# Performance work log

Measured on AMD Instinct MI355X. Metric: run time of the kernel, lower is better.

Reference implementation:

```python
import jax, jax.numpy as jnp
import numpy as np

NUM_ENT = 50000
NUM_REL = 200          # init_rel has 2*NUM_REL rows (fwd + inverse)
D = 200                # init_dim = gcn_dim = embed_dim
B = 1024
E_HALF = 250000        # edges per direction; total 2*E_HALF
PERM = 1
K_H, K_W = 20, 10      # 2*k_w*k_h == 2*embed_dim
NUM_FILT = 96
KER = 9
FLAT_SZ = K_H * 2 * K_W * NUM_FILT * PERM  # 38400


def _bn(x, g, b, axes):
    # batch-norm with batch statistics (training-mode math, no running stats)
    m = jnp.mean(x, axes, keepdims=True)
    v = jnp.var(x, axes, keepdims=True)
    return (x - m) * jax.lax.rsqrt(v + 1e-5) * g + b


def setup_inputs() -> dict:
    key = jax.random.key(0)
    ks = jax.random.split(key, 24)
    rng = np.random.default_rng(0)
    # graph (constants)
    s = jax.random.randint(ks[0], (E_HALF,), 0, NUM_ENT)
    d = jax.random.randint(ks[1], (E_HALF,), 0, NUM_ENT)
    t = jax.random.randint(ks[2], (E_HALF,), 0, NUM_REL)
    edge_index = jnp.stack([jnp.concatenate([s, d]), jnp.concatenate([d, s])])  # [2, 2*E_HALF]
    edge_type = jnp.concatenate([t, t + NUM_REL])
    chequer_perm = jnp.asarray(np.stack([rng.permutation(2 * D) for _ in range(PERM)]), dtype=jnp.int32)
    # batch indices
    sub = jax.random.randint(ks[3], (B,), 0, NUM_ENT)
    rel = jax.random.randint(ks[4], (B,), 0, 2 * NUM_REL)
    neg_ents = jax.random.randint(ks[5], (B,), 0, NUM_ENT)
    n = lambda k, shp, sc=0.05: jax.random.normal(ks[k], shp, jnp.float32) * sc
    return {
        'sub': sub, 'rel': rel, 'neg_ents': neg_ents,
        'edge_index': edge_index, 'edge_type': edge_type, 'chequer_perm': chequer_perm,
        'init_embed': n(6, (NUM_ENT, D)),
        'init_rel': n(7, (2 * NUM_REL, D)),
        'w_in': n(8, (D, D)), 'w_out': n(9, (D, D)), 'w_loop': n(10, (D, D)),
        'w_rel': n(11, (D, D)), 'loop_rel': n(12, (1, D)),
        'bn0_g': jnp.ones((PERM,)), 'bn0_b': jnp.zeros((PERM,)),
        'bn1_g': jnp.ones((NUM_FILT * PERM,)), 'bn1_b': jnp.zeros((NUM_FILT * PERM,)),
        'bn2_g': jnp.ones((D,)), 'bn2_b': jnp.zeros((D,)),
        'conv_filt': n(13, (NUM_FILT, 1, KER, KER), 0.1),
        'fc_w': n(14, (D, FLAT_SZ), 0.01), 'fc_b': jnp.zeros((D,)),
        'bias_ent': jnp.zeros((NUM_ENT,)),
    }


def _forward(init_embed, init_rel, w_in, w_out, w_loop, w_rel, loop_rel,
             bn0_g, bn0_b, bn1_g, bn1_b, bn2_g, bn2_b,
             conv_filt, fc_w, fc_b, bias_ent,
             sub, rel, edge_index, edge_type, chequer_perm):
    # ---- GPKGConv encoder (CompGCN-style, op='sub', eval mode -> dropout off) ----
    src, dst = edge_index[0], edge_index[1]
    msg = init_embed[src] - init_rel[edge_type]                      # [E, D] irregular gather
    msg = jnp.concatenate([msg[:E_HALF] @ w_in, msg[E_HALF:] @ w_out], axis=0)
    deg = jax.ops.segment_sum(jnp.ones(msg.shape[0], msg.dtype), dst, num_segments=NUM_ENT)
    dinv = jnp.where(deg > 0, jax.lax.rsqrt(jnp.maximum(deg, 1.0)), 0.0)
    norm = (dinv[src] * dinv[dst])[:, None]
    agg = jax.ops.segment_sum(msg * norm, dst, num_segments=NUM_ENT)  # irregular scatter
    loop_msg = (init_embed - loop_rel) @ w_loop
    all_ent = jnp.tanh((agg + loop_msg) / 3.0)                        # [num_ent, D]
    r = init_rel @ w_rel                                              # [2*num_rel, D]
    # ---- InteractE-style chequer conv decoder ----
    sub_emb = all_ent[sub]
    rel_emb = r[rel]
    comb = jnp.concatenate([sub_emb, rel_emb], axis=1)                # [B, 2D]
    cheq = jnp.take(comb, chequer_perm, axis=1)                       # [B, perm, 2D]
    x = cheq.reshape(-1, PERM, 2 * K_W, K_H)
    x = _bn(x, bn0_g.reshape(1, -1, 1, 1), bn0_b.reshape(1, -1, 1, 1), (0, 2, 3))
    pad = KER // 2
    x = jnp.pad(x, ((0, 0), (0, 0), (pad, pad), (pad, pad)), mode='wrap')  # circular pad
    filt = jnp.tile(conv_filt, (PERM, 1, 1, 1))
    x = jax.lax.conv_general_dilated(x, filt, (1, 1), 'VALID',
                                     dimension_numbers=('NCHW', 'OIHW', 'NCHW'),
                                     feature_group_count=PERM)        # [B, 96, 20, 20]
    x = _bn(x, bn1_g.reshape(1, -1, 1, 1), bn1_b.reshape(1, -1, 1, 1), (0, 2, 3))
    x = jax.nn.relu(x)
    x = x.reshape(x.shape[0], -1) @ fc_w.T + fc_b                     # [B, D]
    x = _bn(x, bn2_g, bn2_b, (0,))
    x = jax.nn.relu(x)
    logits = x @ all_ent.T + bias_ent                                 # [B, num_ent]
    return jax.nn.sigmoid(logits)


def reference(sub, rel, neg_ents, edge_index, edge_type, chequer_perm,
              init_embed, init_rel, w_in, w_out, w_loop, w_rel, loop_rel,
              bn0_g, bn0_b, bn1_g, bn1_b, bn2_g, bn2_b,
              conv_filt, fc_w, fc_b, bias_ent):
    return _forward(init_embed, init_rel, w_in, w_out, w_loop, w_rel, loop_rel,
                    bn0_g, bn0_b, bn1_g, bn1_b, bn2_g, bn2_b,
                    conv_filt, fc_w, fc_b, bias_ent,
                    sub, rel, edge_index, edge_type, chequer_perm)
```

## Files before the change

kernel.cpp:

```cpp
#include <hip/hip_runtime.h>

#define ETOT  500000
#define EHALF 250000
#define NENT  50000
#define NSEG  (2 * NENT)
#define DD    200
#define BB    1024
#define NF    96
#define FLAT  38400

#define FC_KS     20
#define FC_KSLICE 1920
#define FC_NCHUNK 60

#define LE 64

#define OFF_AGG      0LL
#define ZSTART       20000000LL
#define OFF_CNT      20000000LL
#define OFF_ACC0     20100004LL
#define OFF_ACC1     20100006LL
#define ZEND         20100198LL
#define OFF_CURSOR   20304998LL
#define OFF_BSUM     20404998LL
#define OFF_ELIST    20405126LL
#define OFF_WT       20405128LL
#define OFF_DINV     20905126LL
#define OFF_RMAT     20955126LL
#define OFF_CHEQ     21035126LL
#define OFF_BN1S     21444726LL
#define OFF_X2H      21649720LL
#define OFF_X2L      21752120LL

#define OD_CONV 0LL
#define OD_FWH  39321600LL
#define OD_FWL  43161600LL
#define OD_PART 47001600LL

typedef __attribute__((ext_vector_type(8))) short bf16x8;
typedef __attribute__((ext_vector_type(4))) float f32x4;

__device__ inline void bf16split(float v, ushort& h, ushort& l) {
    unsigned u = __float_as_uint(v);
    unsigned hu = u & 0xffff0000u;
    h = (ushort)(hu >> 16);
    float lf = v - __uint_as_float(hu);
    l = (ushort)(__float_as_uint(lf) >> 16);
}

__device__ inline void split8(const float* e, bf16x8& h8, bf16x8& l8) {
#pragma unroll
    for (int t = 0; t < 8; t++) {
        ushort h, l;
        bf16split(e[t], h, l);
        h8[t] = (short)h;
        l8[t] = (short)l;
    }
}


__global__ void k_hist(const int* __restrict__ ei, int* __restrict__ cnt) {
    int e = blockIdx.x * 256 + threadIdx.x;
    if (e < ETOT) {
        int seg = (e < EHALF ? 0 : NENT) + ei[ETOT + e];
        atomicAdd(&cnt[seg], 1);
    }
}

__global__ void k_dinv(const int* __restrict__ cnt, float* __restrict__ dinv) {
    int i = blockIdx.x * 256 + threadIdx.x;
    if (i < NENT) {
        int d = cnt[i] + cnt[NENT + i];
        dinv[i] = d > 0 ? rsqrtf((float)d) : 0.f;
    }
}

__global__ void k_scan1(int* __restrict__ cnt, int* __restrict__ bsum) {
    __shared__ int S[256];
    int base = blockIdx.x * 1024 + threadIdx.x * 4;
    int v[4], s = 0;
#pragma unroll
    for (int i = 0; i < 4; i++) { v[i] = (base + i <= NSEG) ? cnt[base + i] : 0; s += v[i]; }
    S[threadIdx.x] = s;
    __syncthreads();
    for (int off = 1; off < 256; off <<= 1) {
        int t = (threadIdx.x >= off) ? S[threadIdx.x - off] : 0;
        __syncthreads();
        S[threadIdx.x] += t;
        __syncthreads();
    }
    int run = S[threadIdx.x] - s;
#pragma unroll
    for (int i = 0; i < 4; i++) {
        if (base + i <= NSEG) cnt[base + i] = run;
        run += v[i];
    }
    if (threadIdx.x == 255) bsum[blockIdx.x] = S[255];
}

__global__ void k_scan2(int* __restrict__ bsum) {
    __shared__ int S[128];
    int v = (threadIdx.x < 98) ? bsum[threadIdx.x] : 0;
    S[threadIdx.x] = v;
    __syncthreads();
    for (int off = 1; off < 128; off <<= 1) {
        int t = (threadIdx.x >= off) ? S[threadIdx.x - off] : 0;
        __syncthreads();
        S[threadIdx.x] += t;
        __syncthreads();
    }
    if (threadIdx.x < 98) bsum[threadIdx.x] = S[threadIdx.x] - v;
}

__global__ void k_scan3(int* __restrict__ cnt, const int* __restrict__ bsum,
                        int* __restrict__ cursor) {
    int add = bsum[blockIdx.x];
    int base = blockIdx.x * 1024 + threadIdx.x * 4;
#pragma unroll
    for (int i = 0; i < 4; i++) {
        int idx = base + i;
        if (idx <= NSEG) {
            int v = cnt[idx] + add;
            cnt[idx] = v;
            if (idx < NSEG) cursor[idx] = v;
        }
    }
}

__global__ void k_fill(const int* __restrict__ ei, int* __restrict__ cursor,
                       int* __restrict__ elist) {
    int e = blockIdx.x * 256 + threadIdx.x;
    if (e < ETOT) {
        int seg = (e < EHALF ? 0 : NENT) + ei[ETOT + e];
        int pos = atomicAdd(&cursor[seg], 1);
        elist[pos] = e;
    }
}

__global__ void k_agg(const int* __restrict__ ei, const int* __restrict__ et,
                      const int* __restrict__ row_start, const int* __restrict__ elist,
                      const float* __restrict__ emb, const float* __restrict__ rel,
                      const float* __restrict__ dinv, float* __restrict__ agg) {
    int seg = blockIdx.x * 4 + (threadIdx.x >> 6);
    int lane = threadIdx.x & 63;
    int dst = seg - (seg >= NENT ? NENT : 0);
    float dd = dinv[dst];
    int s = row_start[seg], e = row_start[seg + 1];
    bool act = lane < 50;
    float4 acc = {0.f, 0.f, 0.f, 0.f};
    for (int i = s; i < e; i++) {
        int ed = elist[i];
        int src = ei[ed];
        int t = et[ed];
        float nrm = dinv[src] * dd;
        if (act) {
            float4 a = *(const float4*)&emb[(long long)src * DD + lane * 4];
            float4 b = *(const float4*)&rel[t * DD + lane * 4];
            acc.x += (a.x - b.x) * nrm;
            acc.y += (a.y - b.y) * nrm;
            acc.z += (a.z - b.z) * nrm;
            acc.w += (a.w - b.w) * nrm;
        }
    }
    if (act) *(float4*)&agg[(long long)seg * DD + lane * 4] = acc;
}


__global__ void k_cvt3w(const float* __restrict__ w_in, const float* __restrict__ w_out,
                        const float* __restrict__ w_loop,
                        ushort* __restrict__ wth, ushort* __restrict__ wtl) {
    int idx = blockIdx.x * 256 + threadIdx.x;
    if (idx >= 3 * DD * DD) return;
    int s = idx / (DD * DD);
    int rem = idx - s * DD * DD;
    int j = rem / DD, k = rem - (rem / DD) * DD;
    const float* w = (s == 0) ? w_in : (s == 1) ? w_out : w_loop;
    ushort h, l;
    bf16split(w[k * DD + j], h, l);
    wth[idx] = h;
    wtl[idx] = l;
}

__global__ __launch_bounds__(256) void k_allent_mfma(
        const float* __restrict__ agg, const float* __restrict__ emb,
        const float* __restrict__ loop_rel,
        const ushort* __restrict__ wth, const ushort* __restrict__ wtl,
        float* __restrict__ all_ent) {
    __shared__ float lr[DD];
    int tid = threadIdx.x;
    for (int i = tid; i < DD; i += 256) lr[i] = loop_rel[i];
    __syncthreads();
    int wid = tid >> 6, lane = tid & 63, l15 = lane & 15, q = lane >> 4;
    int r0 = blockIdx.x * 64;
    int nh = blockIdx.y;
    int row = r0 + wid * 16 + l15;
    if (row > NENT - 1) row = NENT - 1;
    const float* apa = &agg[(long long)row * DD];
    const float* apb = &agg[(long long)(NENT + row) * DD];
    const float* apc = &emb[(long long)row * DD];

    int brow[7];
#pragma unroll
    for (int n = 0; n < 7; n++) {
        int j = nh * 112 + n * 16 + l15;
        brow[n] = (j < DD ? j : DD - 1) * DD;
    }

    f32x4 zero4 = {0.f, 0.f, 0.f, 0.f};
    bf16x8 zf = {0, 0, 0, 0, 0, 0, 0, 0};
    f32x4 acc[7];
#pragma unroll
    for (int n = 0; n < 7; n++) acc[n] = zero4;

    float4 a1, a2;
    {
        int k0 = q * 8;
        a1 = *(const float4*)&apa[k0];
        a2 = *(const float4*)&apa[k0 + 4];
    }

    for (int t = 0; t < 21; t++) {
        int s = t / 7, kk = t - s * 7;
        bool prt = (kk == 6);
        int k0 = prt ? 192 : kk * 32 + q * 8;
        bool act = !prt || (q == 0);
        const ushort* bhb = wth + s * (DD * DD);
        const ushort* blb = wtl + s * (DD * DD);
        bf16x8 bh[7], bl[7];
#pragma unroll
        for (int n = 0; n < 7; n++) {
            bh[n] = act ? *(const bf16x8*)&bhb[brow[n] + k0] : zf;
            bl[n] = act ? *(const bf16x8*)&blb[brow[n] + k0] : zf;
        }
        float4 n1 = {0.f, 0.f, 0.f, 0.f}, n2 = {0.f, 0.f, 0.f, 0.f};
        if (t + 1 < 21) {
            int s2 = (t + 1) / 7, kk2 = (t + 1) - s2 * 7;
            bool p2 = (kk2 == 6);
            int k2 = p2 ? 192 : kk2 * 32 + q * 8;
            const float* apn = (s2 == 0) ? apa : (s2 == 1) ? apb : apc;
            if (!p2 || q == 0) {
                n1 = *(const float4*)&apn[k2];
                n2 = *(const float4*)&apn[k2 + 4];
            }
        }
        float e[8] = {0.f, 0.f, 0.f, 0.f, 0.f, 0.f, 0.f, 0.f};
        if (act) {
            float4 v1 = a1, v2 = a2;
            if (s == 2) {
                float4 w1 = *(const float4*)&lr[k0];
                float4 w2 = *(const float4*)&lr[k0 + 4];
                v1.x -= w1.x; v1.y -= w1.y; v1.z -= w1.z; v1.w -= w1.w;
                v2.x -= w2.x; v2.y -= w2.y; v2.z -= w2.z; v2.w -= w2.w;
            }
            e[0] = v1.x; e[1] = v1.y; e[2] = v1.z; e[3] = v1.w;
            e[4] = v2.x; e[5] = v2.y; e[6] = v2.z; e[7] = v2.w;
        }
        bf16x8 ah, al;
        split8(e, ah, al);
#pragma unroll
        for (int n = 0; n < 7; n++) {
            acc[n] = __builtin_amdgcn_mfma_f32_16x16x32_bf16(ah, bh[n], acc[n], 0, 0, 0);
            acc[n] = __builtin_amdgcn_mfma_f32_16x16x32_bf16(ah, bl[n], acc[n], 0, 0, 0);
            acc[n] = __builtin_amdgcn_mfma_f32_16x16x32_bf16(al, bh[n], acc[n], 0, 0, 0);
        }
        a1 = n1; a2 = n2;
    }
#pragma unroll
    for (int n = 0; n < 7; n++) {
        int j = nh * 112 + n * 16 + l15;
        if (j < DD) {
            int rowb = r0 + wid * 16 + q * 4;
#pragma unroll
            for (int r = 0; r < 4; r++) {
                if (rowb + r < NENT)
                    all_ent[(long long)(rowb + r) * DD + j] = tanhf(acc[n][r] * (1.f / 3.f));
            }
        }
    }
}

__global__ void k_cvt(const float* __restrict__ src, ushort* __restrict__ hi,
                      ushort* __restrict__ lo) {
    long long i = (long long)(blockIdx.x * 256 + threadIdx.x) * 4;
    if (i >= (long long)NENT * DD) return;
    float4 v = *(const float4*)&src[i];
    ushort4 h, l;
    bf16split(v.x, h.x, l.x);
    bf16split(v.y, h.y, l.y);
    bf16split(v.z, h.z, l.z);
    bf16split(v.w, h.w, l.w);
    *(ushort4*)&hi[i] = h;
    *(ushort4*)&lo[i] = l;
}

__global__ void k_cvtw(const float* __restrict__ src, ushort* __restrict__ hi,
                       ushort* __restrict__ lo) {
    long long i = (long long)(blockIdx.x * 256 + threadIdx.x) * 4;
    if (i >= (long long)DD * FLAT) return;
    float4 v = *(const float4*)&src[i];
    ushort4 h, l;
    bf16split(v.x, h.x, l.x);
    bf16split(v.y, h.y, l.y);
    bf16split(v.z, h.z, l.z);
    bf16split(v.w, h.w, l.w);
    *(ushort4*)&hi[i] = h;
    *(ushort4*)&lo[i] = l;
}

__global__ void k_rmat(const float* __restrict__ init_rel, const float* __restrict__ w_rel,
                       float* __restrict__ rmat) {
    __shared__ float S[16][DD];
    int r0 = blockIdx.x * 16;
    for (int i = threadIdx.x; i < 16 * DD; i += 256)
        S[i / DD][i % DD] = init_rel[(r0 + i / DD) * DD + i % DD];
    __syncthreads();
    int j = threadIdx.x;
    if (j < DD) {
        float acc[16];
#pragma unroll
        for (int rr = 0; rr < 16; rr++) acc[rr] = 0.f;
        for (int k = 0; k < DD; k += 4) {
            float wx = w_rel[(k + 0) * DD + j], wy = w_rel[(k + 1) * DD + j],
                  wz = w_rel[(k + 2) * DD + j], ww = w_rel[(k + 3) * DD + j];
#pragma unroll
            for (int rr = 0; rr < 16; rr++) {
                float4 a = *(const float4*)&S[rr][k];
                acc[rr] += a.x * wx + a.y * wy + a.z * wz + a.w * ww;
            }
        }
#pragma unroll
        for (int rr = 0; rr < 16; rr++) rmat[(r0 + rr) * DD + j] = acc[rr];
    }
}


__global__ void k_cheq(const int* __restrict__ sub, const int* __restrict__ rel,
                       const int* __restrict__ perm, const float* __restrict__ all_ent,
                       const float* __restrict__ rmat, float* __restrict__ cheq,
                       float* __restrict__ acc0) {
    int i = blockIdx.x * 256 + threadIdx.x;
    int b = i / 400, p = i % 400;
    int c = perm[p];
    float v = (c < DD) ? all_ent[(long long)sub[b] * DD + c]
                       : rmat[rel[b] * DD + (c - DD)];
    cheq[i] = v;
    __shared__ float s1[256], s2[256];
    s1[threadIdx.x] = v;
    s2[threadIdx.x] = v * v;
    __syncthreads();
    for (int st = 128; st > 0; st >>= 1) {
        if (threadIdx.x < st) { s1[threadIdx.x] += s1[threadIdx.x + st]; s2[threadIdx.x] += s2[threadIdx.x + st]; }
        __syncthreads();
    }
    if (threadIdx.x == 0) { atomicAdd(&acc0[0], s1[0]); atomicAdd(&acc0[1], s2[0]); }
}

__global__ void k_conv(const float* __restrict__ cheq, const float* __restrict__ acc0,
                       const float* __restrict__ bn0_g, const float* __restrict__ bn0_b,
                       const float* __restrict__ filt, float* __restrict__ conv_out,
                       float* __restrict__ acc1) {
    __shared__ __align__(16) float xp[28][36];
    __shared__ float fl[NF * 81];
    __shared__ float csum[NF], csq[NF];
    int b = blockIdx.x;
    const float invN = 1.f / (BB * 400.f);
    float mean = acc0[0] * invN;
    float var = acc0[1] * invN - mean * mean;
    float sc = rsqrtf(var + 1e-5f) * bn0_g[0];
    float sh = bn0_b[0] - mean * sc;
    for (int i = threadIdx.x; i < 28 * 28; i += 256) {
        int r = i / 28, c = i % 28;
        int rr = (r + 16) % 20, cc = (c + 16) % 20;
        xp[r][c] = cheq[b * 400 + rr * 20 + cc] * sc + sh;
    }
    for (int i = threadIdx.x; i < NF * 81; i += 256) fl[i] = filt[i];
    if (threadIdx.x < NF) { csum[threadIdx.x] = 0.f; csq[threadIdx.x] = 0.f; }
    __syncthreads();
    for (int t = threadIdx.x; t < NF * 20; t += 256) {
        int ch = t / 20, row = t % 20;
        float acc[20];
#pragma unroll
        for (int c2 = 0; c2 < 20; c2++) acc[c2] = 0.f;
        for (int di = 0; di < 9; di++) {
            float xr[28];
#pragma unroll
            for (int g = 0; g < 7; g++) {
                float4 v = *(const float4*)&xp[row + di][g * 4];
                xr[g * 4 + 0] = v.x; xr[g * 4 + 1] = v.y;
                xr[g * 4 + 2] = v.z; xr[g * 4 + 3] = v.w;
            }
            float f[9];
#pragma unroll
            for (int dj = 0; dj < 9; dj++) f[dj] = fl[ch * 81 + di * 9 + dj];
#pragma unroll
            for (int dj = 0; dj < 9; dj++)
#pragma unroll
                for (int c2 = 0; c2 < 20; c2++)
                    acc[c2] = fmaf(xr[c2 + dj], f[dj], acc[c2]);
        }
        float s = 0.f, q = 0.f;
        long long base = (long long)b * FLAT + ch * 400 + row * 20;
#pragma unroll
        for (int c2 = 0; c2 < 20; c2++) {
            float v = acc[c2];
            s += v; q += v * v;
            conv_out[base + c2] = v;
        }
        atomicAdd(&csum[ch], s);
        atomicAdd(&csq[ch], q);
    }
    __syncthreads();
    if (threadIdx.x < NF) {
        atomicAdd(&acc1[threadIdx.x], csum[threadIdx.x]);
        atomicAdd(&acc1[NF + threadIdx.x], csq[threadIdx.x]);
    }
}

__global__ void k_bn1fin(const float* __restrict__ acc1, const float* __restrict__ g1,
                         const float* __restrict__ b1, float* __restrict__ bn1s) {
    int c = threadIdx.x;
    if (c >= NF) return;
    const float invN = 1.f / (BB * 400.f);
    float m = acc1[c] * invN;
    float v = acc1[NF + c] * invN - m * m;
    float sc = rsqrtf(v + 1e-5f) * g1[c];
    bn1s[c] = sc;
    bn1s[NF + c] = b1[c] - m * sc;
}

__global__ __launch_bounds__(256) void k_fc_mfma(
        const float* __restrict__ conv_out, const float* __restrict__ bn1s,
        const ushort* __restrict__ fwh, const ushort* __restrict__ fwl,
        float* __restrict__ part) {
    __shared__ __align__(16) ushort Bh[2][112][36];
    __shared__ __align__(16) ushort Bl[2][112][36];
    __shared__ float bns[192];
    int tid = threadIdx.x;
    for (int i = tid; i < 192; i += 256) bns[i] = bn1s[i];
    int wid = tid >> 6, lane = tid & 63, l15 = lane & 15, q = lane >> 4;
    int b0 = blockIdx.x * 64;
    int nh = blockIdx.y;
    int ksl = blockIdx.z;
    int kbase = ksl * FC_KSLICE;

    const float* ap = conv_out + (long long)(b0 + wid * 16 + l15) * FLAT;

    bool stg = tid < 224;
    int srow = tid - (tid >= 112 ? 112 : 0);
    if (srow > 111) srow = 0;
    bool spl = (tid >= 112) && stg;
    int sj = nh * 112 + srow;
    int sjr = sj < DD ? sj : DD - 1;
    const ushort* bsrc = (spl ? fwl : fwh) + (long long)sjr * FLAT + kbase;
    ushort* d0 = spl ? &Bl[0][srow][0] : &Bh[0][srow][0];
    ushort* d1 = spl ? &Bl[1][srow][0] : &Bh[1][srow][0];

    f32x4 zero4 = {0.f, 0.f, 0.f, 0.f};
    f32x4 acc[7];
#pragma unroll
    for (int n = 0; n < 7; n++) acc[n] = zero4;

    uint4 s0 = {0u,0u,0u,0u}, s1 = {0u,0u,0u,0u}, s2 = {0u,0u,0u,0u}, s3 = {0u,0u,0u,0u};
    if (stg) {
        s0 = *(const uint4*)&bsrc[0];
        s1 = *(const uint4*)&bsrc[8];
        s2 = *(const uint4*)&bsrc[16];
        s3 = *(const uint4*)&bsrc[24];
        *(uint4*)&d0[0]  = s0;
        *(uint4*)&d0[8]  = s1;
        *(uint4*)&d0[16] = s2;
        *(uint4*)&d0[24] = s3;
    }
    float4 a1, a2;
    {
        int k0 = kbase + q * 8;
        a1 = *(const float4*)&ap[k0];
        a2 = *(const float4*)&ap[k0 + 4];
    }
    __syncthreads();

    for (int c = 0; c < FC_NCHUNK; c++) {
        int buf = c & 1;
        int kc = kbase + c * 32 + q * 8;
        bool more = (c + 1 < FC_NCHUNK);
        if (stg && more) {
            int kn = (c + 1) * 32;
            s0 = *(const uint4*)&bsrc[kn];
            s1 = *(const uint4*)&bsrc[kn + 8];
            s2 = *(const uint4*)&bsrc[kn + 16];
            s3 = *(const uint4*)&bsrc[kn + 24];
        }
        float4 n1 = {0.f, 0.f, 0.f, 0.f}, n2 = {0.f, 0.f, 0.f, 0.f};
        if (more) {
            n1 = *(const float4*)&ap[kc + 32];
            n2 = *(const float4*)&ap[kc + 36];
        }
        int ch = kc / 400;
        float sc = bns[ch], sh = bns[96 + ch];
        float e[8] = {
            fmaxf(a1.x * sc + sh, 0.f), fmaxf(a1.y * sc + sh, 0.f),
            fmaxf(a1.z * sc + sh, 0.f), fmaxf(a1.w * sc + sh, 0.f),
            fmaxf(a2.x * sc + sh, 0.f), fmaxf(a2.y * sc + sh, 0.f),
            fmaxf(a2.z * sc + sh, 0.f), fmaxf(a2.w * sc + sh, 0.f)};
        bf16x8 ah, al;
        split8(e, ah, al);
#pragma unroll
        for (int n = 0; n < 7; n++) {
            bf16x8 bh = *(const bf16x8*)&Bh[buf][n * 16 + l15][q * 8];
            bf16x8 bl = *(const bf16x8*)&Bl[buf][n * 16 + l15][q * 8];
            acc[n] = __builtin_amdgcn_mfma_f32_16x16x32_bf16(ah, bh, acc[n], 0, 0, 0);
            acc[n] = __builtin_amdgcn_mfma_f32_16x16x32_bf16(ah, bl, acc[n], 0, 0, 0);
            acc[n] = __builtin_amdgcn_mfma_f32_16x16x32_bf16(al, bh, acc[n], 0, 0, 0);
        }
        if (stg && more) {
            ushort* d = buf ? d0 : d1;
            *(uint4*)&d[0]  = s0;
            *(uint4*)&d[8]  = s1;
            *(uint4*)&d[16] = s2;
            *(uint4*)&d[24] = s3;
        }
        __syncthreads();
        a1 = n1; a2 = n2;
    }
    long long pbase = (long long)ksl * (BB * DD);
#pragma unroll
    for (int n = 0; n < 7; n++) {
        int j = nh * 112 + n * 16 + l15;
        if (j < DD) {
            int rowb = b0 + wid * 16 + q * 4;
#pragma unroll
            for (int r = 0; r < 4; r++)
                part[pbase + (long long)(rowb + r) * DD + j] = acc[n][r];
        }
    }
}

__global__ void k_bn2(const float* __restrict__ part, const float* __restrict__ fc_b,
                      const float* __restrict__ g2, const float* __restrict__ b2,
                      ushort* __restrict__ x2h, ushort* __restrict__ x2l) {
    int j = blockIdx.x;
    float vals[4];
    float s = 0.f, q = 0.f;
#pragma unroll
    for (int i = 0; i < 4; i++) {
        int b = threadIdx.x + i * 256;
        float v = fc_b[j];
#pragma unroll
        for (int ks = 0; ks < FC_KS; ks++)
            v += part[(long long)ks * (BB * DD) + (long long)b * DD + j];
        vals[i] = v;
        s += v; q += v * v;
    }
    __shared__ float r1[256], r2[256];
    __shared__ float bc[2];
    r1[threadIdx.x] = s; r2[threadIdx.x] = q;
    __syncthreads();
    for (int st = 128; st > 0; st >>= 1) {
        if (threadIdx.x < st) { r1[threadIdx.x] += r1[threadIdx.x + st]; r2[threadIdx.x] += r2[threadIdx.x + st]; }
        __syncthreads();
    }
    if (threadIdx.x == 0) {
        float m = r1[0] * (1.f / BB);
        float v = r2[0] * (1.f / BB) - m * m;
        float sc = rsqrtf(v + 1e-5f) * g2[j];
        bc[0] = sc; bc[1] = b2[j] - m * sc;
    }
    __syncthreads();
    float sc = bc[0], sh = bc[1];
#pragma unroll
    for (int i = 0; i < 4; i++) {
        int b = threadIdx.x + i * 256;
        float v = fmaxf(vals[i] * sc + sh, 0.f);
        ushort h, l;
        bf16split(v, h, l);
        x2h[b * DD + j] = h;
        x2l[b * DD + j] = l;
    }
}

__global__ __launch_bounds__(512) void k_logits_mfma(
        const ushort* __restrict__ x2h, const ushort* __restrict__ x2l,
        const ushort* __restrict__ aeh, const ushort* __restrict__ ael,
        const float* __restrict__ bias, float* __restrict__ out) {
    __shared__ ushort Bhs[LE * DD];
    __shared__ ushort Bls[LE * DD];
    int e0 = blockIdx.x * LE;
    for (int i = threadIdx.x; i < 2 * LE * 25; i += 512) {
        int pl = i >= LE * 25;
        int ii = pl ? i - LE * 25 : i;
        int row = ii / 25, seg = ii % 25;
        int e = e0 + row;
        if (e > NENT - 1) e = NENT - 1;
        const ushort* src = (pl ? ael : aeh) + (long long)e * DD + seg * 8;
        uint4 v = *(const uint4*)src;
        if (pl) *(uint4*)&Bls[row * DD + seg * 8] = v;
        else    *(uint4*)&Bhs[row * DD + seg * 8] = v;
    }
    __syncthreads();

    int wid = threadIdx.x >> 6;
    int lane = threadIdx.x & 63;
    int l15 = lane & 15, q = lane >> 4;
    int wm = wid >> 1;
    int wn = wid & 1;

    float bv0, bv1;
    bool ev0, ev1;
    int e_0 = e0 + wn * 32 + l15;
    int e_1 = e0 + wn * 32 + 16 + l15;
    ev0 = e_0 < NENT; ev1 = e_1 < NENT;
    bv0 = bias[ev0 ? e_0 : NENT - 1];
    bv1 = bias[ev1 ? e_1 : NENT - 1];
    int nbase0 = (wn * 32 + l15) * DD;
    int nbase1 = (wn * 32 + 16 + l15) * DD;

    f32x4 zero4 = {0.f, 0.f, 0.f, 0.f};
    bf16x8 zf = {0, 0, 0, 0, 0, 0, 0, 0};
    const int STEP = 128 * DD;

    const ushort* ah0 = x2h + (long long)(wm * 32 + l15) * DD;
    const ushort* al0 = x2l + (long long)(wm * 32 + l15) * DD;
    const ushort* ah1 = ah0 + 16 * DD;
    const ushort* al1 = al0 + 16 * DD;

    bf16x8 pa_h0, pa_l0, pa_h1, pa_l1;
    {
        int k0 = q * 8;
        pa_h0 = *(const bf16x8*)&ah0[k0];
        pa_l0 = *(const bf16x8*)&al0[k0];
        pa_h1 = *(const bf16x8*)&ah1[k0];
        pa_l1 = *(const bf16x8*)&al1[k0];
    }

    for (int it = 0; it < 8; it++) {
        f32x4 acc00 = zero4, acc01 = zero4, acc10 = zero4, acc11 = zero4;
#pragma unroll
        for (int kk = 0; kk < 6; kk++) {
            int kn = (kk < 5) ? (kk + 1) * 32 + q * 8 : 192;
            bf16x8 na_h0 = *(const bf16x8*)&ah0[kn];
            bf16x8 na_l0 = *(const bf16x8*)&al0[kn];
            bf16x8 na_h1 = *(const bf16x8*)&ah1[kn];
            bf16x8 na_l1 = *(const bf16x8*)&al1[kn];
            int kb = kk * 32 + q * 8;
            bf16x8 bh0 = *(const bf16x8*)&Bhs[nbase0 + kb];
            bf16x8 bl0 = *(const bf16x8*)&Bls[nbase0 + kb];
            bf16x8 bh1 = *(const bf16x8*)&Bhs[nbase1 + kb];
            bf16x8 bl1 = *(const bf16x8*)&Bls[nbase1 + kb];
            acc00 = __builtin_amdgcn_mfma_f32_16x16x32_bf16(pa_h0, bh0, acc00, 0, 0, 0);
            acc00 = __builtin_amdgcn_mfma_f32_16x16x32_bf16(pa_h0, bl0, acc00, 0, 0, 0);
            acc00 = __builtin_amdgcn_mfma_f32_16x16x32_bf16(pa_l0, bh0, acc00, 0, 0, 0);
            acc01 = __builtin_amdgcn_mfma_f32_16x16x32_bf16(pa_h0, bh1, acc01, 0, 0, 0);
            acc01 = __builtin_amdgcn_mfma_f32_16x16x32_bf16(pa_h0, bl1, acc01, 0, 0, 0);
            acc01 = __builtin_amdgcn_mfma_f32_16x16x32_bf16(pa_l0, bh1, acc01, 0, 0, 0);
            acc10 = __builtin_amdgcn_mfma_f32_16x16x32_bf16(pa_h1, bh0, acc10, 0, 0, 0);
            acc10 = __builtin_amdgcn_mfma_f32_16x16x32_bf16(pa_h1, bl0, acc10, 0, 0, 0);
            acc10 = __builtin_amdgcn_mfma_f32_16x16x32_bf16(pa_l1, bh0, acc10, 0, 0, 0);
            acc11 = __builtin_amdgcn_mfma_f32_16x16x32_bf16(pa_h1, bh1, acc11, 0, 0, 0);
            acc11 = __builtin_amdgcn_mfma_f32_16x16x32_bf16(pa_h1, bl1, acc11, 0, 0, 0);
            acc11 = __builtin_amdgcn_mfma_f32_16x16x32_bf16(pa_l1, bh1, acc11, 0, 0, 0);
            pa_h0 = na_h0; pa_l0 = na_l0; pa_h1 = na_h1; pa_l1 = na_l1;
        }
        {
            bf16x8 na_h0 = zf, na_l0 = zf, na_h1 = zf, na_l1 = zf;
            if (it + 1 < 8) {
                int k0 = q * 8;
                na_h0 = *(const bf16x8*)&ah0[STEP + k0];
                na_l0 = *(const bf16x8*)&al0[STEP + k0];
                na_h1 = *(const bf16x8*)&ah1[STEP + k0];
                na_l1 = *(const bf16x8*)&al1[STEP + k0];
            }
            bool a0 = (q == 0);
            bf16x8 xh0 = a0 ? pa_h0 : zf, xl0 = a0 ? pa_l0 : zf;
            bf16x8 xh1 = a0 ? pa_h1 : zf, xl1 = a0 ? pa_l1 : zf;
            bf16x8 bh0 = a0 ? *(const bf16x8*)&Bhs[nbase0 + 192] : zf;
            bf16x8 bl0 = a0 ? *(const bf16x8*)&Bls[nbase0 + 192] : zf;
            bf16x8 bh1 = a0 ? *(const bf16x8*)&Bhs[nbase1 + 192] : zf;
            bf16x8 bl1 = a0 ? *(const bf16x8*)&Bls[nbase1 + 192] : zf;
            acc00 = __builtin_amdgcn_mfma_f32_16x16x32_bf16(xh0, bh0, acc00, 0, 0, 0);
            acc00 = __builtin_amdgcn_mfma_f32_16x16x32_bf16(xh0, bl0, acc00, 0, 0, 0);
            acc00 = __builtin_amdgcn_mfma_f32_16x16x32_bf16(xl0, bh0, acc00, 0, 0, 0);
            acc01 = __builtin_amdgcn_mfma_f32_16x16x32_bf16(xh0, bh1, acc01, 0, 0, 0);
            acc01 = __builtin_amdgcn_mfma_f32_16x16x32_bf16(xh0, bl1, acc01, 0, 0, 0);
            acc01 = __builtin_amdgcn_mfma_f32_16x16x32_bf16(xl0, bh1, acc01, 0, 0, 0);
            acc10 = __builtin_amdgcn_mfma_f32_16x16x32_bf16(xh1, bh0, acc10, 0, 0, 0);
            acc10 = __builtin_amdgcn_mfma_f32_16x16x32_bf16(xh1, bl0, acc10, 0, 0, 0);
            acc10 = __builtin_amdgcn_mfma_f32_16x16x32_bf16(xl1, bh0, acc10, 0, 0, 0);
            acc11 = __builtin_amdgcn_mfma_f32_16x16x32_bf16(xh1, bh1, acc11, 0, 0, 0);
            acc11 = __builtin_amdgcn_mfma_f32_16x16x32_bf16(xh1, bl1, acc11, 0, 0, 0);
            acc11 = __builtin_amdgcn_mfma_f32_16x16x32_bf16(xl1, bh1, acc11, 0, 0, 0);
            pa_h0 = na_h0; pa_l0 = na_l0; pa_h1 = na_h1; pa_l1 = na_l1;
        }
        int rb0 = it * 128 + wm * 32 + q * 4;
        int rb1 = rb0 + 16;
        if (ev0) {
#pragma unroll
            for (int r = 0; r < 4; r++) {
                float t0 = acc00[r] + bv0;
                out[(long long)(rb0 + r) * NENT + e_0] = 1.f / (1.f + __expf(-t0));
                float t1 = acc10[r] + bv0;
                out[(long long)(rb1 + r) * NENT + e_0] = 1.f / (1.f + __expf(-t1));
            }
        }
        if (ev1) {
#pragma unroll
            for (int r = 0; r < 4; r++) {
                float t0 = acc01[r] + bv1;
                out[(long long)(rb0 + r) * NENT + e_1] = 1.f / (1.f + __expf(-t0));
                float t1 = acc11[r] + bv1;
                out[(long long)(rb1 + r) * NENT + e_1] = 1.f / (1.f + __expf(-t1));
            }
        }
        ah0 += STEP; al0 += STEP; ah1 += STEP; al1 += STEP;
    }
}


extern "C" void kernel_launch(void* const* d_in, const int* in_sizes, int n_in,
                              void* d_out, int out_size, void* d_ws, size_t ws_size,
                              hipStream_t stream) {
    const int*   sub      = (const int*)d_in[0];
    const int*   rel      = (const int*)d_in[1];
    const int*   ei       = (const int*)d_in[3];
    const int*   et       = (const int*)d_in[4];
    const int*   perm     = (const int*)d_in[5];
    const float* emb      = (const float*)d_in[6];
    const float* init_rel = (const float*)d_in[7];
    const float* w_in     = (const float*)d_in[8];
    const float* w_out    = (const float*)d_in[9];
    const float* w_loop   = (const float*)d_in[10];
    const float* w_rel    = (const float*)d_in[11];
    const float* loop_rel = (const float*)d_in[12];
    const float* bn0_g    = (const float*)d_in[13];
    const float* bn0_b    = (const float*)d_in[14];
    const float* bn1_g    = (const float*)d_in[15];
    const float* bn1_b    = (const float*)d_in[16];
    const float* bn2_g    = (const float*)d_in[17];
    const float* bn2_b    = (const float*)d_in[18];
    const float* filt     = (const float*)d_in[19];
    const float* fc_w     = (const float*)d_in[20];
    const float* fc_b     = (const float*)d_in[21];
    const float* bias_ent = (const float*)d_in[22];

    float* ws  = (float*)d_ws;
    float* o   = (float*)d_out;

    float* agg     = ws + OFF_AGG;
    float* agg_out = agg + (long long)NENT * DD;
    int*   cnt     = (int*)(ws + OFF_CNT);
    int*   cursor  = (int*)(ws + OFF_CURSOR);
    int*   bsum    = (int*)(ws + OFF_BSUM);
    int*   elist   = (int*)(ws + OFF_ELIST);
    ushort* wth    = (ushort*)(ws + OFF_WT);
    ushort* wtl    = wth + 3 * DD * DD;
    float* acc0    = ws + OFF_ACC0;
    float* acc1    = ws + OFF_ACC1;
    float* dinv    = ws + OFF_DINV;
    float* rmat    = ws + OFF_RMAT;
    float* cheq    = ws + OFF_CHEQ;
    float* bn1s    = ws + OFF_BN1S;
    ushort* x2h    = (ushort*)(ws + OFF_X2H);
    ushort* x2l    = (ushort*)(ws + OFF_X2L);
    ushort* aeh    = (ushort*)agg_out;
    ushort* ael    = aeh + (long long)NENT * DD;

    float*  all_ent  = o + OD_CONV;
    float*  conv_out = o + OD_CONV;
    ushort* fwh      = (ushort*)(o + OD_FWH);
    ushort* fwl      = (ushort*)(o + OD_FWL);
    float*  part     = o + OD_PART;

    hipMemsetAsync(ws + ZSTART, 0, (size_t)(ZEND - ZSTART) * 4, stream);

    k_hist<<<(ETOT + 255) / 256, 256, 0, stream>>>(ei, cnt);
    k_dinv<<<(NENT + 255) / 256, 256, 0, stream>>>(cnt, dinv);
    k_scan1<<<98, 256, 0, stream>>>(cnt, bsum);
    k_scan2<<<1, 128, 0, stream>>>(bsum);
    k_scan3<<<98, 256, 0, stream>>>(cnt, bsum, cursor);
    k_fill<<<(ETOT + 255) / 256, 256, 0, stream>>>(ei, cursor, elist);
    k_agg<<<NSEG / 4, 256, 0, stream>>>(ei, et, cnt, elist, emb, init_rel, dinv, agg);

    k_cvt3w<<<(3 * DD * DD + 255) / 256, 256, 0, stream>>>(w_in, w_out, w_loop, wth, wtl);
    k_allent_mfma<<<dim3((NENT + 63) / 64, 2), 256, 0, stream>>>(agg, emb, loop_rel,
                                                                 wth, wtl, all_ent);
    k_cvt<<<((NENT * DD / 4) + 255) / 256, 256, 0, stream>>>(all_ent, aeh, ael);
    k_cvtw<<<((DD * FLAT / 4) + 255) / 256, 256, 0, stream>>>(fc_w, fwh, fwl);
    k_rmat<<<400 / 16, 256, 0, stream>>>(init_rel, w_rel, rmat);

    k_cheq<<<(BB * 400) / 256, 256, 0, stream>>>(sub, rel, perm, all_ent, rmat, cheq, acc0);
    k_conv<<<BB, 256, 0, stream>>>(cheq, acc0, bn0_g, bn0_b, filt, conv_out, acc1);
    k_bn1fin<<<1, 128, 0, stream>>>(acc1, bn1_g, bn1_b, bn1s);
    k_fc_mfma<<<dim3(BB / 64, 2, FC_KS), 256, 0, stream>>>(conv_out, bn1s, fwh, fwl, part);
    k_bn2<<<DD, 256, 0, stream>>>(part, fc_b, bn2_g, bn2_b, x2h, x2l);
    k_logits_mfma<<<(NENT + LE - 1) / LE, 512, 0, stream>>>(
        x2h, x2l, aeh, ael, bias_ent, o);
}
```

Baseline: 909.7 us.

## Stage weight tiles through double-buffered LDS in all-entity MFMA kernel

Each of the four waves previously loaded its B-operand weight fragments (hi and lo bf16 planes) straight from global memory, so the same weights were fetched four times per block. Now 224 threads cooperatively stage a 112x32 slice of each plane into a double-buffered shared-memory tile, prefetching the next k-step into registers while the MFMAs run. This cuts redundant global and L2 traffic for the weights. In exchange it adds a block-wide barrier per k-step and more LDS use, which may lower occupancy.

```diff
diff --git a/kernel.cpp b/kernel.cpp
--- a/kernel.cpp
+++ b/kernel.cpp
@@ -186,10 +186,11 @@
         const float* __restrict__ loop_rel,
         const ushort* __restrict__ wth, const ushort* __restrict__ wtl,
         float* __restrict__ all_ent) {
+    __shared__ __align__(16) ushort Bh[2][112][36];
+    __shared__ __align__(16) ushort Bl[2][112][36];
     __shared__ float lr[DD];
     int tid = threadIdx.x;
     for (int i = tid; i < DD; i += 256) lr[i] = loop_rel[i];
-    __syncthreads();
     int wid = tid >> 6, lane = tid & 63, l15 = lane & 15, q = lane >> 4;
     int r0 = blockIdx.x * 64;
     int nh = blockIdx.y;
@@ -199,58 +200,79 @@
     const float* apb = &agg[(long long)(NENT + row) * DD];
     const float* apc = &emb[(long long)row * DD];
 
-    int brow[7];
-#pragma unroll
-    for (int n = 0; n < 7; n++) {
-        int j = nh * 112 + n * 16 + l15;
-        brow[n] = (j < DD ? j : DD - 1) * DD;
-    }
+    bool stg = tid < 224;
+    int srow = tid - (tid >= 112 ? 112 : 0);
+    if (srow > 111) srow = 0;
+    bool spl = (tid >= 112) && stg;
+    int sj = nh * 112 + srow;
+    int sjr = sj < DD ? sj : DD - 1;
+    const ushort* bplane = spl ? wtl : wth;
+    int srowoff = sjr * DD;
+    ushort* d0 = spl ? &Bl[0][srow][0] : &Bh[0][srow][0];
+    ushort* d1 = spl ? &Bl[1][srow][0] : &Bh[1][srow][0];
 
     f32x4 zero4 = {0.f, 0.f, 0.f, 0.f};
-    bf16x8 zf = {0, 0, 0, 0, 0, 0, 0, 0};
     f32x4 acc[7];
 #pragma unroll
     for (int n = 0; n < 7; n++) acc[n] = zero4;
 
+    uint4 w0 = {0u,0u,0u,0u}, w1 = {0u,0u,0u,0u}, w2 = {0u,0u,0u,0u}, w3 = {0u,0u,0u,0u};
+    if (stg) {
+        const ushort* src = bplane + srowoff;
+        w0 = *(const uint4*)&src[0];
+        w1 = *(const uint4*)&src[8];
+        w2 = *(const uint4*)&src[16];
+        w3 = *(const uint4*)&src[24];
+        *(uint4*)&d0[0]  = w0;
+        *(uint4*)&d0[8]  = w1;
+        *(uint4*)&d0[16] = w2;
+        *(uint4*)&d0[24] = w3;
+    }
     float4 a1, a2;
     {
         int k0 = q * 8;
         a1 = *(const float4*)&apa[k0];
         a2 = *(const float4*)&apa[k0 + 4];
     }
+    __syncthreads();
 
     for (int t = 0; t < 21; t++) {
+        int buf = t & 1;
         int s = t / 7, kk = t - s * 7;
         bool prt = (kk == 6);
         int k0 = prt ? 192 : kk * 32 + q * 8;
         bool act = !prt || (q == 0);
-        const ushort* bhb = wth + s * (DD * DD);
-        const ushort* blb = wtl + s * (DD * DD);
-        bf16x8 bh[7], bl[7];
-#pragma unroll
-        for (int n = 0; n < 7; n++) {
-            bh[n] = act ? *(const bf16x8*)&bhb[brow[n] + k0] : zf;
-            bl[n] = act ? *(const bf16x8*)&blb[brow[n] + k0] : zf;
+        bool more = (t + 1 < 21);
+        if (stg && more) {
+            int t2 = t + 1, ss = t2 / 7, k2 = t2 - ss * 7;
+            bool p2 = (k2 == 6);
+            int koff2 = p2 ? 192 : k2 * 32;
+            const ushort* src = bplane + ss * (DD * DD) + srowoff + koff2;
+            uint4 zz = {0u,0u,0u,0u};
+            w0 = *(const uint4*)&src[0];
+            w1 = p2 ? zz : *(const uint4*)&src[8];
+            w2 = p2 ? zz : *(const uint4*)&src[16];
+            w3 = p2 ? zz : *(const uint4*)&src[24];
         }
         float4 n1 = {0.f, 0.f, 0.f, 0.f}, n2 = {0.f, 0.f, 0.f, 0.f};
-        if (t + 1 < 21) {
-            int s2 = (t + 1) / 7, kk2 = (t + 1) - s2 * 7;
-            bool p2 = (kk2 == 6);
-            int k2 = p2 ? 192 : kk2 * 32 + q * 8;
-            const float* apn = (s2 == 0) ? apa : (s2 == 1) ? apb : apc;
+        if (more) {
+            int t2 = t + 1, ss = t2 / 7, k2 = t2 - ss * 7;
+            bool p2 = (k2 == 6);
+            int ka = p2 ? 192 : k2 * 32 + q * 8;
+            const float* apn = (ss == 0) ? apa : (ss == 1) ? apb : apc;
             if (!p2 || q == 0) {
-                n1 = *(const float4*)&apn[k2];
-                n2 = *(const float4*)&apn[k2 + 4];
+                n1 = *(const float4*)&apn[ka];
+                n2 = *(const float4*)&apn[ka + 4];
             }
         }
         float e[8] = {0.f, 0.f, 0.f, 0.f, 0.f, 0.f, 0.f, 0.f};
         if (act) {
             float4 v1 = a1, v2 = a2;
             if (s == 2) {
-                float4 w1 = *(const float4*)&lr[k0];
-                float4 w2 = *(const float4*)&lr[k0 + 4];
-                v1.x -= w1.x; v1.y -= w1.y; v1.z -= w1.z; v1.w -= w1.w;
-                v2.x -= w2.x; v2.y -= w2.y; v2.z -= w2.z; v2.w -= w2.w;
+                float4 u1 = *(const float4*)&lr[k0];
+                float4 u2 = *(const float4*)&lr[k0 + 4];
+                v1.x -= u1.x; v1.y -= u1.y; v1.z -= u1.z; v1.w -= u1.w;
+                v2.x -= u2.x; v2.y -= u2.y; v2.z -= u2.z; v2.w -= u2.w;
             }
             e[0] = v1.x; e[1] = v1.y; e[2] = v1.z; e[3] = v1.w;
             e[4] = v2.x; e[5] = v2.y; e[6] = v2.z; e[7] = v2.w;
@@ -259,10 +281,20 @@
         split8(e, ah, al);
 #pragma unroll
         for (int n = 0; n < 7; n++) {
-            acc[n] = __builtin_amdgcn_mfma_f32_16x16x32_bf16(ah, bh[n], acc[n], 0, 0, 0);
-            acc[n] = __builtin_amdgcn_mfma_f32_16x16x32_bf16(ah, bl[n], acc[n], 0, 0, 0);
-            acc[n] = __builtin_amdgcn_mfma_f32_16x16x32_bf16(al, bh[n], acc[n], 0, 0, 0);
-        }
+            bf16x8 bh = *(const bf16x8*)&Bh[buf][n * 16 + l15][q * 8];
+            bf16x8 bl = *(const bf16x8*)&Bl[buf][n * 16 + l15][q * 8];
+            acc[n] = __builtin_amdgcn_mfma_f32_16x16x32_bf16(ah, bh, acc[n], 0, 0, 0);
+            acc[n] = __builtin_amdgcn_mfma_f32_16x16x32_bf16(ah, bl, acc[n], 0, 0, 0);
+            acc[n] = __builtin_amdgcn_mfma_f32_16x16x32_bf16(al, bh, acc[n], 0, 0, 0);
+        }
+        if (stg && more) {
+            ushort* d = buf ? d0 : d1;
+            *(uint4*)&d[0]  = w0;
+            *(uint4*)&d[8]  = w1;
+            *(uint4*)&d[16] = w2;
+            *(uint4*)&d[24] = w3;
+        }
+        __syncthreads();
         a1 = n1; a2 = n2;
     }
 #pragma unroll
```

New measurement: 846.9 us. 6.9% less time.
